# Kernel tuning notes

Hardware: AMD Instinct MI355X
Metric: run time of the kernel (lower is better)

Reference implementation:

```python
import jax, jax.numpy as jnp
import numpy as np

N = 8192
IN_F = 128
OUT_F = 64
NEG_SLOPE = 0.2


def setup_inputs() -> dict:
    key = jax.random.key(0)
    k1, k2, k3, k4 = jax.random.split(key, 4)
    x = jax.random.normal(k1, (N, IN_F), dtype=jnp.float32)
    adj = jax.random.randint(k2, (N, N), 0, 2, dtype=jnp.int32)
    W = jax.random.normal(k3, (IN_F, OUT_F), dtype=jnp.float32) * (1.414 / np.sqrt(IN_F))
    a = jax.random.normal(k4, (2 * OUT_F, 1), dtype=jnp.float32) * 0.5
    return {"x": x, "adj": adj, "W": W, "a": a}


def reference(x, adj, W, a):
    # Wh: [N, F]
    Wh = x @ W
    # Decomposed pairwise score: e_ij = leaky_relu(Wh_i . a1 + Wh_j . a2)
    # identical math to the original [N*N, 2F] concat @ a construction.
    a1 = a[:OUT_F, 0]   # [F]
    a2 = a[OUT_F:, 0]   # [F]
    s1 = Wh @ a1        # [N]
    s2 = Wh @ a2        # [N]
    e = jax.nn.leaky_relu(s1[:, None] + s2[None, :], negative_slope=NEG_SLOPE)  # [N, N]
    # NOTE: the original zeros out non-edges (NOT -inf) before softmax.
    att = jnp.where(adj > 0, e, jnp.zeros_like(e))
    att = jax.nn.softmax(att, axis=1)
    return att @ Wh  # [N, F]
```

## Files before the change

kernel.cpp:

```cpp
#include <hip/hip_runtime.h>
#include <hip/hip_bf16.h>

#define N_NODES 8192
#define IN_FEAT 128
#define OUT_FEAT 64
#define NEG_SLOPE 0.2f
#define TILES (N_NODES / 16)
#define CCH 2
#define COLS (N_NODES / CCH)
#define SUBC 512
#define NSUB (COLS / SUBC)
#define KPW 4
#define ROWPAD 528
#define BUFSZ (16 * ROWPAD)
#define LOG2E 1.44269504088896340736f

using f32x4  = __attribute__((ext_vector_type(4))) float;
using i32x4  = __attribute__((ext_vector_type(4))) int;
using bf16x8 = __attribute__((ext_vector_type(8))) short;

static __device__ __forceinline__ short f2bf(float f) {
    unsigned int u = __float_as_uint(f);
    unsigned int r = (u + 0x7FFFu + ((u >> 16) & 1u)) >> 16;
    return (short)r;
}

static __device__ __forceinline__ short f2bf_fast(float f) {
    __hip_bfloat16 h = __float2bfloat16(f);
    return __builtin_bit_cast(short, h);
}

static __device__ __forceinline__ float exp2_fast(float x) {
    return __builtin_amdgcn_exp2f(x);
}

__global__ __launch_bounds__(256) void k_wh(
    const float* __restrict__ x, const float* __restrict__ W,
    const float* __restrict__ a,
    float* __restrict__ s1, float* __restrict__ s2,
    unsigned short* __restrict__ whb)
{
    __shared__ float xs[4][IN_FEAT];
    const int wv   = threadIdx.x >> 6;
    const int lane = threadIdx.x & 63;
    const int row  = blockIdx.x * 4 + wv;

    const float2 xv = *(const float2*)(x + (size_t)row * IN_FEAT + lane * 2);
    xs[wv][lane * 2]     = xv.x;
    xs[wv][lane * 2 + 1] = xv.y;
    __syncthreads();

    float acc = 0.f;
    #pragma unroll
    for (int k = 0; k < IN_FEAT; ++k)
        acc = fmaf(xs[wv][k], W[k * OUT_FEAT + lane], acc);

    float p1 = acc * a[lane];
    float p2 = acc * a[OUT_FEAT + lane];
    #pragma unroll
    for (int off = 32; off; off >>= 1) {
        p1 += __shfl_xor(p1, off);
        p2 += __shfl_xor(p2, off);
    }
    if (lane == 0) {
        s1[row] = p1 * LOG2E;
        s2[row] = p2 * LOG2E;
    }

    const int jb = row >> 5;
    const int ri = row & 31;
    const int gl = ri >> 3;
    const int e  = ri & 7;
    const int fg = lane >> 4;
    const int cl = lane & 15;
    whb[(((size_t)(jb * 4 + fg) * 64) + (gl * 16 + cl)) * 8 + e] = (unsigned short)f2bf(acc);
}

__global__ __launch_bounds__(256, 4) void k_fused(
    const int* __restrict__ adj, const float* __restrict__ s1v,
    const float* __restrict__ s2v, const unsigned short* __restrict__ whb,
    float* __restrict__ pnum, float* __restrict__ pz)
{
    __shared__ __align__(16) char lds[2 * BUFSZ + COLS * 4 + 256];
    char*  bufs = lds;
    float* s2l  = (float*)(lds + 2 * BUFSZ);
    float* zl   = (float*)(lds + 2 * BUFSZ + COLS * 4);
    float* red  = (float*)lds;

    const int lane = threadIdx.x & 63;
    const int w    = threadIdx.x >> 6;
    const int tile = blockIdx.x;
    const int cidx = blockIdx.y;
    const int c0   = cidx * COLS;
    const int cl = lane & 15, g = lane >> 4;
    const int row = tile * 16 + cl;
    const float s1r = s1v[row];

    const int* stg = adj + ((size_t)(tile * 16 + w * 4)) * N_NODES + c0 + lane * 4;

    i32x4 ld[8];

    auto issue = [&](int c) {
        #pragma unroll
        for (int rr = 0; rr < 4; ++rr)
            #pragma unroll
            for (int q = 0; q < 2; ++q)
                ld[rr * 2 + q] = __builtin_nontemporal_load(
                    (const i32x4*)(stg + (size_t)rr * N_NODES + c * SUBC + q * 256));
    };
    auto pack = [&](int c) {
        char* wbuf = bufs + (c & 1) * BUFSZ;
        #pragma unroll
        for (int rr = 0; rr < 4; ++rr)
            #pragma unroll
            for (int q = 0; q < 2; ++q) {
                i32x4 v = ld[rr * 2 + q];
                unsigned int d = (v[0] > 0 ? 1u : 0u) | (v[1] > 0 ? 0x100u : 0u)
                               | (v[2] > 0 ? 0x10000u : 0u) | (v[3] > 0 ? 0x1000000u : 0u);
                *(unsigned int*)(wbuf + (w * 4 + rr) * ROWPAD + q * 256 + lane * 4) = d;
            }
    };

    f32x4 acc0 = {0.f, 0.f, 0.f, 0.f};
    f32x4 acc1 = acc0, acc2 = acc0, acc3 = acc0;
    float zacc = 0.f;

    auto compute = [&](int c) {
        const char* rbuf = bufs + (c & 1) * BUFSZ;
        #pragma unroll
        for (int kk = 0; kk < KPW; ++kk) {
            const int ks = w * KPW + kk;
            const uint2 ab = *(const uint2*)(rbuf + cl * ROWPAD + ks * 32 + 8 * g);
            const float* sp = s2l + c * SUBC + ks * 32 + 8 * g;
            const f32x4 s0  = *(const f32x4*)(sp);
            const f32x4 s1x = *(const f32x4*)(sp + 4);
            const unsigned short* wq =
                whb + ((size_t)(c0 / 32 + c * 16 + ks)) * 2048 + lane * 8;
            bf16x8 B0 = *(const bf16x8*)(wq);
            bf16x8 B1 = *(const bf16x8*)(wq + 512);
            bf16x8 B2 = *(const bf16x8*)(wq + 1024);
            bf16x8 B3 = *(const bf16x8*)(wq + 1536);

            bf16x8 af;
            #pragma unroll
            for (int e = 0; e < 4; ++e) {
                float tv = s1r + s0[e];
                float el = fmaxf(tv, NEG_SLOPE * tv);
                float wv = ((ab.x >> (8 * e)) & 1u) ? exp2_fast(el) : 1.0f;
                zacc += wv;
                af[e] = f2bf_fast(wv);
            }
            #pragma unroll
            for (int e = 0; e < 4; ++e) {
                float tv = s1r + s1x[e];
                float el = fmaxf(tv, NEG_SLOPE * tv);
                float wv = ((ab.y >> (8 * e)) & 1u) ? exp2_fast(el) : 1.0f;
                zacc += wv;
                af[4 + e] = f2bf_fast(wv);
            }

            acc0 = __builtin_amdgcn_mfma_f32_16x16x32_bf16(af, B0, acc0, 0, 0, 0);
            acc1 = __builtin_amdgcn_mfma_f32_16x16x32_bf16(af, B1, acc1, 0, 0, 0);
            acc2 = __builtin_amdgcn_mfma_f32_16x16x32_bf16(af, B2, acc2, 0, 0, 0);
            acc3 = __builtin_amdgcn_mfma_f32_16x16x32_bf16(af, B3, acc3, 0, 0, 0);
        }
    };

    {
        const float* src = s2v + c0 + threadIdx.x * 4;
        float* dst = s2l + threadIdx.x * 4;
        #pragma unroll
        for (int i = 0; i < 4; ++i)
            *(f32x4*)(dst + i * 1024) = *(const f32x4*)(src + i * 1024);
    }
    issue(0);
    pack(0);
    issue(1);
    __builtin_amdgcn_sched_barrier(0);
    asm volatile("s_waitcnt lgkmcnt(0)" ::: "memory");
    __builtin_amdgcn_s_barrier();
    __builtin_amdgcn_sched_barrier(0);

    for (int c = 0; c < NSUB; ++c) {
        if (c + 1 < NSUB) pack(c + 1);
        __builtin_amdgcn_sched_barrier(0);
        if (c + 2 < NSUB) issue(c + 2);
        __builtin_amdgcn_sched_barrier(0);
        compute(c);
        __builtin_amdgcn_sched_barrier(0);
        asm volatile("s_waitcnt lgkmcnt(0)" ::: "memory");
        __builtin_amdgcn_s_barrier();
        __builtin_amdgcn_sched_barrier(0);
    }

    *(f32x4*)(red + ((size_t)(w * 64 + lane)) * 16 + 0)  = acc0;
    *(f32x4*)(red + ((size_t)(w * 64 + lane)) * 16 + 4)  = acc1;
    *(f32x4*)(red + ((size_t)(w * 64 + lane)) * 16 + 8)  = acc2;
    *(f32x4*)(red + ((size_t)(w * 64 + lane)) * 16 + 12) = acc3;
    float zz = zacc + __shfl_xor(zacc, 16);
    zz += __shfl_xor(zz, 32);
    if (lane < 16) zl[w * 16 + lane] = zz;
    __syncthreads();

    f32x4 rs = {0.f, 0.f, 0.f, 0.f};
    #pragma unroll
    for (int w2 = 0; w2 < 4; ++w2)
        rs += *(const f32x4*)(red + ((size_t)(w2 * 64 + lane)) * 16 + 4 * w);

    float* pb = pnum + ((size_t)cidx * TILES + tile) * 16 * 64 + lane;
    #pragma unroll
    for (int q = 0; q < 4; ++q) pb[(w * 4 + q) * 64] = rs[q];

    if (w == 0 && lane < 16) {
        float z = zl[lane] + zl[16 + lane] + zl[32 + lane] + zl[48 + lane];
        pz[(size_t)cidx * N_NODES + tile * 16 + lane] = z;
    }
}

__global__ __launch_bounds__(64) void k_out(
    const float* __restrict__ pnum, const float* __restrict__ pz,
    float* __restrict__ out)
{
    const int lane = threadIdx.x;
    const int tile = blockIdx.x;
    const int nt   = blockIdx.y;
    const int g = lane >> 4, cli = lane & 15;

    float acc[4] = {0.f, 0.f, 0.f, 0.f};
    float zz[4]  = {0.f, 0.f, 0.f, 0.f};
    #pragma unroll
    for (int c = 0; c < CCH; ++c) {
        const float* pb = pnum + (((size_t)c * TILES + tile) * 16 + nt * 4) * 64 + lane;
        #pragma unroll
        for (int q = 0; q < 4; ++q) acc[q] += pb[q * 64];
        const float* zb = pz + (size_t)c * N_NODES + tile * 16 + g * 4;
        #pragma unroll
        for (int q = 0; q < 4; ++q) zz[q] += zb[q];
    }
    #pragma unroll
    for (int q = 0; q < 4; ++q) {
        const int node = tile * 16 + g * 4 + q;
        out[(size_t)node * OUT_FEAT + nt * 16 + cli] = acc[q] / zz[q];
    }
}

extern "C" void kernel_launch(void* const* d_in, const int* in_sizes, int n_in,
                              void* d_out, int out_size, void* d_ws, size_t ws_size,
                              hipStream_t stream) {
    const float* x   = (const float*)d_in[0];
    const int*   adj = (const int*)d_in[1];
    const float* W   = (const float*)d_in[2];
    const float* a   = (const float*)d_in[3];
    float* out = (float*)d_out;

    char* ws = (char*)d_ws;
    float* s1 = (float*)(ws);
    float* s2 = (float*)(ws + 32 * 1024);
    unsigned short* whb = (unsigned short*)(ws + 64 * 1024);
    float* pnum = (float*)(ws + 2u * 1024 * 1024);
    float* pz   = (float*)(ws + 8u * 1024 * 1024);

    k_wh   <<<dim3(N_NODES / 4), dim3(256), 0, stream>>>(x, W, a, s1, s2, whb);
    k_fused<<<dim3(TILES, CCH), dim3(256), 0, stream>>>(adj, s1, s2, whb, pnum, pz);
    k_out  <<<dim3(TILES, 4), dim3(64), 0, stream>>>(pnum, pz, out);
}
```

Before: 87.51 us.

## Warp-specialize fused kernel into loader and compute waves, drop column split

Each block now has 512 threads: four waves only stream and pack the adjacency rows into LDS, while four other waves run the exp/MFMA compute, synchronised by block barriers. Every block covers all 8192 columns of its 16-row tile, so the partial numerator/denominator buffers and the separate k_out reduction kernel go away and the block writes the normalised output directly. The goal is to overlap the HBM adjacency stream with compute and to cut a kernel launch plus the partial-sum traffic. In exchange the grid halves to 512 blocks, the s2 LDS buffer doubles to 32 KB, and the producer/consumer barrier counts have to match exactly.

New measurement: 85.73 us. 2.0% less time.

```diff
diff --git a/kernel.cpp b/kernel.cpp
--- a/kernel.cpp
+++ b/kernel.cpp
@@ -6,10 +6,8 @@
 #define OUT_FEAT 64
 #define NEG_SLOPE 0.2f
 #define TILES (N_NODES / 16)
-#define CCH 2
-#define COLS (N_NODES / CCH)
 #define SUBC 512
-#define NSUB (COLS / SUBC)
+#define NSUB (N_NODES / SUBC)
 #define KPW 4
 #define ROWPAD 528
 #define BUFSZ (16 * ROWPAD)
@@ -76,171 +74,150 @@
     whb[(((size_t)(jb * 4 + fg) * 64) + (gl * 16 + cl)) * 8 + e] = (unsigned short)f2bf(acc);
 }
 
-__global__ __launch_bounds__(256, 4) void k_fused(
+__global__ __launch_bounds__(512, 4) void k_fused(
     const int* __restrict__ adj, const float* __restrict__ s1v,
     const float* __restrict__ s2v, const unsigned short* __restrict__ whb,
-    float* __restrict__ pnum, float* __restrict__ pz)
+    float* __restrict__ out)
 {
-    __shared__ __align__(16) char lds[2 * BUFSZ + COLS * 4 + 256];
+    __shared__ __align__(16) char lds[2 * BUFSZ + N_NODES * 4 + 256];
     char*  bufs = lds;
     float* s2l  = (float*)(lds + 2 * BUFSZ);
-    float* zl   = (float*)(lds + 2 * BUFSZ + COLS * 4);
+    float* zl   = (float*)(lds + 2 * BUFSZ + N_NODES * 4);
     float* red  = (float*)lds;
 
-    const int lane = threadIdx.x & 63;
-    const int w    = threadIdx.x >> 6;
+    const int tid  = threadIdx.x;
+    const int lane = tid & 63;
+    const int w    = tid >> 6;
     const int tile = blockIdx.x;
-    const int cidx = blockIdx.y;
-    const int c0   = cidx * COLS;
     const int cl = lane & 15, g = lane >> 4;
-    const int row = tile * 16 + cl;
-    const float s1r = s1v[row];
-
-    const int* stg = adj + ((size_t)(tile * 16 + w * 4)) * N_NODES + c0 + lane * 4;
-
-    i32x4 ld[8];
-
-    auto issue = [&](int c) {
-        #pragma unroll
-        for (int rr = 0; rr < 4; ++rr)
-            #pragma unroll
-            for (int q = 0; q < 2; ++q)
-                ld[rr * 2 + q] = __builtin_nontemporal_load(
-                    (const i32x4*)(stg + (size_t)rr * N_NODES + c * SUBC + q * 256));
-    };
-    auto pack = [&](int c) {
-        char* wbuf = bufs + (c & 1) * BUFSZ;
-        #pragma unroll
-        for (int rr = 0; rr < 4; ++rr)
-            #pragma unroll
-            for (int q = 0; q < 2; ++q) {
-                i32x4 v = ld[rr * 2 + q];
-                unsigned int d = (v[0] > 0 ? 1u : 0u) | (v[1] > 0 ? 0x100u : 0u)
-                               | (v[2] > 0 ? 0x10000u : 0u) | (v[3] > 0 ? 0x1000000u : 0u);
-                *(unsigned int*)(wbuf + (w * 4 + rr) * ROWPAD + q * 256 + lane * 4) = d;
-            }
-    };
-
-    f32x4 acc0 = {0.f, 0.f, 0.f, 0.f};
-    f32x4 acc1 = acc0, acc2 = acc0, acc3 = acc0;
-    float zacc = 0.f;
-
-    auto compute = [&](int c) {
-        const char* rbuf = bufs + (c & 1) * BUFSZ;
-        #pragma unroll
-        for (int kk = 0; kk < KPW; ++kk) {
-            const int ks = w * KPW + kk;
-            const uint2 ab = *(const uint2*)(rbuf + cl * ROWPAD + ks * 32 + 8 * g);
-            const float* sp = s2l + c * SUBC + ks * 32 + 8 * g;
-            const f32x4 s0  = *(const f32x4*)(sp);
-            const f32x4 s1x = *(const f32x4*)(sp + 4);
-            const unsigned short* wq =
-                whb + ((size_t)(c0 / 32 + c * 16 + ks)) * 2048 + lane * 8;
-            bf16x8 B0 = *(const bf16x8*)(wq);
-            bf16x8 B1 = *(const bf16x8*)(wq + 512);
-            bf16x8 B2 = *(const bf16x8*)(wq + 1024);
-            bf16x8 B3 = *(const bf16x8*)(wq + 1536);
-
-            bf16x8 af;
-            #pragma unroll
-            for (int e = 0; e < 4; ++e) {
-                float tv = s1r + s0[e];
-                float el = fmaxf(tv, NEG_SLOPE * tv);
-                float wv = ((ab.x >> (8 * e)) & 1u) ? exp2_fast(el) : 1.0f;
-                zacc += wv;
-                af[e] = f2bf_fast(wv);
-            }
-            #pragma unroll
-            for (int e = 0; e < 4; ++e) {
-                float tv = s1r + s1x[e];
-                float el = fmaxf(tv, NEG_SLOPE * tv);
-                float wv = ((ab.y >> (8 * e)) & 1u) ? exp2_fast(el) : 1.0f;
-                zacc += wv;
-                af[4 + e] = f2bf_fast(wv);
-            }
-
-            acc0 = __builtin_amdgcn_mfma_f32_16x16x32_bf16(af, B0, acc0, 0, 0, 0);
-            acc1 = __builtin_amdgcn_mfma_f32_16x16x32_bf16(af, B1, acc1, 0, 0, 0);
-            acc2 = __builtin_amdgcn_mfma_f32_16x16x32_bf16(af, B2, acc2, 0, 0, 0);
-            acc3 = __builtin_amdgcn_mfma_f32_16x16x32_bf16(af, B3, acc3, 0, 0, 0);
-        }
-    };
 
     {
-        const float* src = s2v + c0 + threadIdx.x * 4;
-        float* dst = s2l + threadIdx.x * 4;
+        const float* src = s2v + tid * 4;
         #pragma unroll
         for (int i = 0; i < 4; ++i)
-            *(f32x4*)(dst + i * 1024) = *(const f32x4*)(src + i * 1024);
-    }
-    issue(0);
-    pack(0);
-    issue(1);
-    __builtin_amdgcn_sched_barrier(0);
-    asm volatile("s_waitcnt lgkmcnt(0)" ::: "memory");
-    __builtin_amdgcn_s_barrier();
-    __builtin_amdgcn_sched_barrier(0);
-
-    for (int c = 0; c < NSUB; ++c) {
-        if (c + 1 < NSUB) pack(c + 1);
-        __builtin_amdgcn_sched_barrier(0);
-        if (c + 2 < NSUB) issue(c + 2);
-        __builtin_amdgcn_sched_barrier(0);
-        compute(c);
-        __builtin_amdgcn_sched_barrier(0);
+            *(f32x4*)(s2l + tid * 4 + i * 2048) = *(const f32x4*)(src + i * 2048);
+    }
+
+    if (w < 4) {
+        const int* stg = adj + ((size_t)(tile * 16 + w * 4)) * N_NODES + lane * 4;
+        i32x4 ldA[8], ldB[8];
+
+        auto issue = [&](i32x4 (&ld)[8], int c) {
+            #pragma unroll
+            for (int rr = 0; rr < 4; ++rr)
+                #pragma unroll
+                for (int q = 0; q < 2; ++q)
+                    ld[rr * 2 + q] = __builtin_nontemporal_load(
+                        (const i32x4*)(stg + (size_t)rr * N_NODES + c * SUBC + q * 256));
+        };
+        auto pack = [&](i32x4 (&ld)[8], int c) {
+            char* wbuf = bufs + (c & 1) * BUFSZ;
+            #pragma unroll
+            for (int rr = 0; rr < 4; ++rr)
+                #pragma unroll
+                for (int q = 0; q < 2; ++q) {
+                    i32x4 v = ld[rr * 2 + q];
+                    unsigned int d = (v[0] > 0 ? 1u : 0u) | (v[1] > 0 ? 0x100u : 0u)
+                                   | (v[2] > 0 ? 0x10000u : 0u) | (v[3] > 0 ? 0x1000000u : 0u);
+                    *(unsigned int*)(wbuf + (w * 4 + rr) * ROWPAD + q * 256 + lane * 4) = d;
+                }
+        };
+
+        issue(ldA, 0);
+        issue(ldB, 1);
+        pack(ldA, 0);
         asm volatile("s_waitcnt lgkmcnt(0)" ::: "memory");
         __builtin_amdgcn_s_barrier();
-        __builtin_amdgcn_sched_barrier(0);
-    }
-
-    *(f32x4*)(red + ((size_t)(w * 64 + lane)) * 16 + 0)  = acc0;
-    *(f32x4*)(red + ((size_t)(w * 64 + lane)) * 16 + 4)  = acc1;
-    *(f32x4*)(red + ((size_t)(w * 64 + lane)) * 16 + 8)  = acc2;
-    *(f32x4*)(red + ((size_t)(w * 64 + lane)) * 16 + 12) = acc3;
-    float zz = zacc + __shfl_xor(zacc, 16);
-    zz += __shfl_xor(zz, 32);
-    if (lane < 16) zl[w * 16 + lane] = zz;
-    __syncthreads();
-
-    f32x4 rs = {0.f, 0.f, 0.f, 0.f};
-    #pragma unroll
-    for (int w2 = 0; w2 < 4; ++w2)
-        rs += *(const f32x4*)(red + ((size_t)(w2 * 64 + lane)) * 16 + 4 * w);
-
-    float* pb = pnum + ((size_t)cidx * TILES + tile) * 16 * 64 + lane;
-    #pragma unroll
-    for (int q = 0; q < 4; ++q) pb[(w * 4 + q) * 64] = rs[q];
-
-    if (w == 0 && lane < 16) {
-        float z = zl[lane] + zl[16 + lane] + zl[32 + lane] + zl[48 + lane];
-        pz[(size_t)cidx * N_NODES + tile * 16 + lane] = z;
-    }
-}
-
-__global__ __launch_bounds__(64) void k_out(
-    const float* __restrict__ pnum, const float* __restrict__ pz,
-    float* __restrict__ out)
-{
-    const int lane = threadIdx.x;
-    const int tile = blockIdx.x;
-    const int nt   = blockIdx.y;
-    const int g = lane >> 4, cli = lane & 15;
-
-    float acc[4] = {0.f, 0.f, 0.f, 0.f};
-    float zz[4]  = {0.f, 0.f, 0.f, 0.f};
-    #pragma unroll
-    for (int c = 0; c < CCH; ++c) {
-        const float* pb = pnum + (((size_t)c * TILES + tile) * 16 + nt * 4) * 64 + lane;
+
+        for (int c = 0; c < NSUB; c += 2) {
+            if (c + 2 < NSUB) issue(ldA, c + 2);
+            __builtin_amdgcn_sched_barrier(0);
+            pack(ldB, c + 1);
+            __builtin_amdgcn_sched_barrier(0);
+            asm volatile("s_waitcnt lgkmcnt(0)" ::: "memory");
+            __builtin_amdgcn_s_barrier();
+            if (c + 3 < NSUB) issue(ldB, c + 3);
+            __builtin_amdgcn_sched_barrier(0);
+            if (c + 2 < NSUB) pack(ldA, c + 2);
+            __builtin_amdgcn_sched_barrier(0);
+            asm volatile("s_waitcnt lgkmcnt(0)" ::: "memory");
+            __builtin_amdgcn_s_barrier();
+        }
+
+        __builtin_amdgcn_s_barrier();
+        f32x4 rs = {0.f, 0.f, 0.f, 0.f};
         #pragma unroll
-        for (int q = 0; q < 4; ++q) acc[q] += pb[q * 64];
-        const float* zb = pz + (size_t)c * N_NODES + tile * 16 + g * 4;
+        for (int w2 = 0; w2 < 4; ++w2)
+            rs += *(const f32x4*)(red + ((size_t)(w2 * 64 + lane)) * 16 + 4 * w);
         #pragma unroll
-        for (int q = 0; q < 4; ++q) zz[q] += zb[q];
-    }
-    #pragma unroll
-    for (int q = 0; q < 4; ++q) {
-        const int node = tile * 16 + g * 4 + q;
-        out[(size_t)node * OUT_FEAT + nt * 16 + cli] = acc[q] / zz[q];
+        for (int q = 0; q < 4; ++q) {
+            const int rit = g * 4 + q;
+            const float z = zl[rit] + zl[16 + rit] + zl[32 + rit] + zl[48 + rit];
+            out[(size_t)(tile * 16 + rit) * OUT_FEAT + w * 16 + cl] = rs[q] / z;
+        }
+    } else {
+        const int cw  = w - 4;
+        const int row = tile * 16 + cl;
+        const float s1r = s1v[row];
+
+        f32x4 acc0 = {0.f, 0.f, 0.f, 0.f};
+        f32x4 acc1 = acc0, acc2 = acc0, acc3 = acc0;
+        float zacc = 0.f;
+
+        asm volatile("s_waitcnt lgkmcnt(0)" ::: "memory");
+        __builtin_amdgcn_s_barrier();
+
+        for (int c = 0; c < NSUB; ++c) {
+            const char* rbuf = bufs + (c & 1) * BUFSZ;
+            #pragma unroll
+            for (int kk = 0; kk < KPW; ++kk) {
+                const int ks = cw * KPW + kk;
+                const uint2 ab = *(const uint2*)(rbuf + cl * ROWPAD + ks * 32 + 8 * g);
+                const float* sp = s2l + c * SUBC + ks * 32 + 8 * g;
+                const f32x4 s0  = *(const f32x4*)(sp);
+                const f32x4 s1x = *(const f32x4*)(sp + 4);
+                const unsigned short* wq = whb + ((size_t)(c * 16 + ks)) * 2048 + lane * 8;
+                bf16x8 B0 = *(const bf16x8*)(wq);
+                bf16x8 B1 = *(const bf16x8*)(wq + 512);
+                bf16x8 B2 = *(const bf16x8*)(wq + 1024);
+                bf16x8 B3 = *(const bf16x8*)(wq + 1536);
+
+                bf16x8 af;
+                #pragma unroll
+                for (int e = 0; e < 4; ++e) {
+                    float tv = s1r + s0[e];
+                    float el = fmaxf(tv, NEG_SLOPE * tv);
+                    float wv = ((ab.x >> (8 * e)) & 1u) ? exp2_fast(el) : 1.0f;
+                    zacc += wv;
+                    af[e] = f2bf_fast(wv);
+                }
+                #pragma unroll
+                for (int e = 0; e < 4; ++e) {
+                    float tv = s1r + s1x[e];
+                    float el = fmaxf(tv, NEG_SLOPE * tv);
+                    float wv = ((ab.y >> (8 * e)) & 1u) ? exp2_fast(el) : 1.0f;
+                    zacc += wv;
+                    af[4 + e] = f2bf_fast(wv);
+                }
+
+                acc0 = __builtin_amdgcn_mfma_f32_16x16x32_bf16(af, B0, acc0, 0, 0, 0);
+                acc1 = __builtin_amdgcn_mfma_f32_16x16x32_bf16(af, B1, acc1, 0, 0, 0);
+                acc2 = __builtin_amdgcn_mfma_f32_16x16x32_bf16(af, B2, acc2, 0, 0, 0);
+                acc3 = __builtin_amdgcn_mfma_f32_16x16x32_bf16(af, B3, acc3, 0, 0, 0);
+            }
+            asm volatile("s_waitcnt lgkmcnt(0)" ::: "memory");
+            __builtin_amdgcn_s_barrier();
+        }
+
+        *(f32x4*)(red + ((size_t)(cw * 64 + lane)) * 16 + 0)  = acc0;
+        *(f32x4*)(red + ((size_t)(cw * 64 + lane)) * 16 + 4)  = acc1;
+        *(f32x4*)(red + ((size_t)(cw * 64 + lane)) * 16 + 8)  = acc2;
+        *(f32x4*)(red + ((size_t)(cw * 64 + lane)) * 16 + 12) = acc3;
+        float zz = zacc + __shfl_xor(zacc, 16);
+        zz += __shfl_xor(zz, 32);
+        if (lane < 16) zl[cw * 16 + lane] = zz;
+        asm volatile("s_waitcnt lgkmcnt(0)" ::: "memory");
+        __builtin_amdgcn_s_barrier();
     }
 }
 
@@ -257,10 +234,7 @@
     float* s1 = (float*)(ws);
     float* s2 = (float*)(ws + 32 * 1024);
     unsigned short* whb = (unsigned short*)(ws + 64 * 1024);
-    float* pnum = (float*)(ws + 2u * 1024 * 1024);
-    float* pz   = (float*)(ws + 8u * 1024 * 1024);
 
     k_wh   <<<dim3(N_NODES / 4), dim3(256), 0, stream>>>(x, W, a, s1, s2, whb);
-    k_fused<<<dim3(TILES, CCH), dim3(256), 0, stream>>>(adj, s1, s2, whb, pnum, pz);
-    k_out  <<<dim3(TILES, 4), dim3(64), 0, stream>>>(pnum, pz, out);
-}
+    k_fused<<<dim3(TILES), dim3(512), 0, stream>>>(adj, s1, s2, whb, out);
+}
```
